# Performance work log

Hardware: AMD Instinct MI355X
Metric: run time of the kernel (lower is better)

The kernel has to match this reference:

```python
import jax, jax.numpy as jnp
import numpy as np

GROUPS = 8   # GroupNorm groups used by create_pat_conv*_blocks(..., groups=8)
EPS = 1e-5
K = 20       # num_neighbor


def group_norm(x, gamma, beta):
    # x: [B, C, ...spatial]
    B, C = x.shape[0], x.shape[1]
    shape = x.shape
    xg = x.reshape(B, GROUPS, C // GROUPS, -1)
    m = xg.mean(axis=(2, 3), keepdims=True)
    v = ((xg - m) ** 2).mean(axis=(2, 3), keepdims=True)
    xg = (xg - m) * jax.lax.rsqrt(v + EPS)
    x = xg.reshape(shape)
    bshape = (1, C) + (1,) * (len(shape) - 2)
    return x * gamma.reshape(bshape) + beta.reshape(bshape)


def conv_block(x, w, b, gamma, beta):
    # pointwise (kernel-size 1) conv + GroupNorm + ELU, works for 1d and 2d spatial
    y = jnp.einsum('oc,bc...->bo...', w, x) + b.reshape((1, -1) + (1,) * (x.ndim - 2))
    return jax.nn.elu(group_norm(y, gamma, beta))


def knn_graph(points, k):
    # points: [B, 3, N] -> neighbor coords [B, 3, N, k] (self included, dilation=1)
    sq = jnp.sum(points * points, axis=1)                      # [B, N]
    inner = jnp.einsum('bci,bcj->bij', points, points)         # [B, N, N]
    dist = sq[:, :, None] + sq[:, None, :] - 2.0 * inner       # squared pairwise dist
    _, idx = jax.lax.top_k(-dist, k)                           # [B, N, k] smallest dists
    neighbors = jnp.take_along_axis(points[:, :, None, :], idx[:, None, :, :], axis=3)
    return neighbors                                           # [B, 3, N, k]


def setup_inputs() -> dict:
    key = jax.random.key(0)
    B, N = 4, 8192
    dims1 = [6, 32, 64]
    dims2 = [64, 512, 1024]
    keys = iter(jax.random.split(key, 32))
    inp = {"points": jax.random.normal(next(keys), (B, 3, N), dtype=jnp.float32)}
    for tag, dims in (("p1", dims1), ("p2", dims2)):
        for i in range(len(dims) - 1):
            cin, cout = dims[i], dims[i + 1]
            inp[f"{tag}_w{i}"] = jax.random.normal(next(keys), (cout, cin), dtype=jnp.float32) / np.float32(np.sqrt(cin))
            inp[f"{tag}_b{i}"] = jnp.zeros((cout,), dtype=jnp.float32)
            inp[f"{tag}_g{i}"] = jnp.ones((cout,), dtype=jnp.float32)
            inp[f"{tag}_beta{i}"] = jnp.zeros((cout,), dtype=jnp.float32)
    return inp


def reference(points, p1_w0, p1_b0, p1_g0, p1_beta0, p1_w1, p1_b1, p1_g1, p1_beta1,
              p2_w0, p2_b0, p2_g0, p2_beta0, p2_w1, p2_b1, p2_g1, p2_beta1):
    neighbors = knn_graph(points, K)                             # [B, 3, N, K]
    center = jnp.broadcast_to(points[:, :, :, None], neighbors.shape)
    x = jnp.concatenate([center, neighbors - center], axis=1)   # [B, 6, N, K]
    x = conv_block(x, p1_w0, p1_b0, p1_g0, p1_beta0)            # [B, 32, N, K]
    x = conv_block(x, p1_w1, p1_b1, p1_g1, p1_beta1)            # [B, 64, N, K]
    x = jnp.max(x, axis=2)                                      # [B, 64, K] (faithful to source: max over dim=2)
    x = conv_block(x, p2_w0, p2_b0, p2_g0, p2_beta0)            # [B, 512, K]
    x = conv_block(x, p2_w1, p2_b1, p2_g1, p2_beta1)            # [B, 1024, K]
    return x
```

## Files before the change

kernel.cpp:

```cpp
#include <hip/hip_runtime.h>
#include <math.h>

#define NPTS   8192
#define BATCH  4
#define KNN    20
#define NKTOT  (NPTS*KNN)
#define EPS    1e-5f
#define FQC    64

#define WINW   3072
#define WITR   (WINW/4/128)
#define GWIN   2048
#define GITR   (GWIN/4/128)
#define NBIN   1024
#define BIN_LO (-4.5f)
#define BIN_W  (9.0f/1024.0f)

typedef float v2f __attribute__((ext_vector_type(2)));

__device__ __forceinline__ float elu(float x) { return x > 0.0f ? x : expm1f(x); }
__device__ __forceinline__ float eluf(float x) { return x > 0.0f ? x : __expf(x) - 1.0f; }
__device__ __forceinline__ v2f splat2(float x) { v2f v; v.x = x; v.y = x; return v; }
__device__ __forceinline__ float rfl(float x) {
    return __uint_as_float(__builtin_amdgcn_readfirstlane(__float_as_uint(x)));
}

__device__ __forceinline__ unsigned fenc(float f) {
    unsigned b = __float_as_uint(f);
    return b ^ ((unsigned)(((int)b) >> 31) | 0x80000000u);
}
__device__ __forceinline__ float fdec(unsigned u) {
    unsigned b = (u & 0x80000000u) ? (u ^ 0x80000000u) : ~u;
    return __uint_as_float(b);
}

__device__ __forceinline__ int xbin(float x) {
    int bin = (int)floorf((x + 4.5f) * (1024.0f / 9.0f));
    return bin < 0 ? 0 : (bin > NBIN - 1 ? NBIN - 1 : bin);
}

__device__ __forceinline__ unsigned long long packkey(float s, int orig, int slot) {
    return ((unsigned long long)fenc(s) << 32)
         | (unsigned)(((NPTS - 1 - orig) << 13) | slot);
}

__global__ __launch_bounds__(256) void prep_kernel(const float* __restrict__ points,
                                                   float4* __restrict__ pts4,
                                                   float* __restrict__ zeroreg,
                                                   unsigned* __restrict__ minenc,
                                                   unsigned* __restrict__ fcnt,
                                                   int* __restrict__ Pcur_part)
{
    __shared__ int lh[NBIN];
    const int t = blockIdx.x * 256 + threadIdx.x;
    const int b = t >> 13, n = t & (NPTS - 1);
    for (int i = threadIdx.x; i < NBIN; i += 256) lh[i] = 0;
    const float* px = points + b * 3 * NPTS;
    float x = px[n], y = px[NPTS + n], z = px[2 * NPTS + n];
    pts4[t] = make_float4(x, y, z, -0.5f * (x * x + y * y + z * z));
    if (t < 18176) zeroreg[t] = 0.f;
    if (t < 5120)  minenc[t] = 0xFFFFFFFFu;
    if (t < 4)     fcnt[t] = 0u;
    __syncthreads();
    atomicAdd(&lh[xbin(x)], 1);
    __syncthreads();
    for (int i = threadIdx.x; i < NBIN; i += 256)
        Pcur_part[blockIdx.x * NBIN + i] = lh[i];
}

__global__ __launch_bounds__(1024) void scan_kernel(const int* __restrict__ Pcur_part,
                                                    int* __restrict__ Pcur)
{
    __shared__ int sc[NBIN];
    const int b = blockIdx.x;
    const int t = threadIdx.x;
    int v = 0;
#pragma unroll 8
    for (int p = 0; p < 32; ++p)
        v += Pcur_part[(b * 32 + p) * NBIN + t];
    sc[t] = v;
    __syncthreads();
    for (int off = 1; off < NBIN; off <<= 1) {
        int a = (t >= off) ? sc[t - off] : 0;
        __syncthreads();
        sc[t] += a;
        __syncthreads();
    }
    Pcur[b * NBIN + t] = sc[t] - v;
}

__global__ __launch_bounds__(256) void scatter_kernel(const float4* __restrict__ pts4,
                                                      int* __restrict__ Pcur,
                                                      float4* __restrict__ psort,
                                                      int* __restrict__ sidx,
                                                      int* __restrict__ binof)
{
    const int t = blockIdx.x * 256 + threadIdx.x;
    const int b = t >> 13, n = t & (NPTS - 1);
    float4 p = pts4[t];
    int bin = xbin(p.x);
    int slot = atomicAdd(&Pcur[b * NBIN + bin], 1);
    psort[b * NPTS + slot] = p;
    sidx [b * NPTS + slot] = n;
    binof[b * NPTS + slot] = bin;
}

__global__ __launch_bounds__(256, 8) void knn_win_kernel(
    const float4* __restrict__ psort, const int* __restrict__ sidx,
    const int* __restrict__ binof, int* __restrict__ idx_out,
    unsigned* __restrict__ fcnt, int* __restrict__ flist)
{
    __shared__ unsigned long long queue[8][FQC];
    __shared__ float smaxs[4][8][64];
    __shared__ float gates[8];
    __shared__ int qcnt[8];

    const int tid  = threadIdx.x;
    const int lane = tid & 63;
    const int wv   = tid >> 6;
    const int b    = blockIdx.x >> 10;
    const int oct  = blockIdx.x & 1023;
    const int q0s  = oct * 8;
    const float4* psb = psort + b * NPTS;
    const int*    six = sidx  + b * NPTS;
    const int*    bob = binof + b * NPTS;

    int s = q0s + 4 - WINW / 2;
    if (s < 0) s = 0;
    if (s > NPTS - WINW) s = NPTS - WINW;
    int gs = q0s + 4 - GWIN / 2;
    if (gs < 0) gs = 0;
    if (gs > NPTS - GWIN) gs = NPTS - GWIN;

    if (tid < 8) qcnt[tid] = 0;

    float qx[8], qy[8], qz[8], q2[8];
    v2f smax2[8];
#pragma unroll
    for (int q = 0; q < 8; ++q) {
        float4 qp = psb[q0s + q];
        qx[q] = rfl(qp.x); qy[q] = rfl(qp.y); qz[q] = rfl(qp.z);
        q2[q] = rfl(-(qp.w + qp.w));
        smax2[q] = splat2(-INFINITY);
    }

    const int gbase = gs + (((lane >> 5) * 4 + wv) << 6) + ((lane & 31) << 1);
    const int lbase = s  + (((lane >> 5) * 4 + wv) << 6) + ((lane & 31) << 1);

#pragma unroll
    for (int t = 0; t < GITR; ++t) {
        float4 p0 = psb[gbase + t * 512];
        float4 p1 = psb[gbase + t * 512 + 1];
        v2f px = { p0.x, p1.x }, py = { p0.y, p1.y };
        v2f pz = { p0.z, p1.z }, pw = { p0.w, p1.w };
#pragma unroll
        for (int q = 0; q < 8; ++q) {
            v2f sv = __builtin_elementwise_fma(splat2(qx[q]), px,
                     __builtin_elementwise_fma(splat2(qy[q]), py,
                     __builtin_elementwise_fma(splat2(qz[q]), pz, pw)));
            smax2[q] = __builtin_elementwise_max(smax2[q], sv);
        }
    }
#pragma unroll
    for (int q = 0; q < 8; ++q) smaxs[wv][q][lane] = fmaxf(smax2[q].x, smax2[q].y);
    __syncthreads();

#pragma unroll
    for (int qq = 0; qq < 2; ++qq) {
        const int q = wv * 2 + qq;
        float v = fmaxf(fmaxf(smaxs[0][q][lane], smaxs[1][q][lane]),
                        fmaxf(smaxs[2][q][lane], smaxs[3][q][lane]));
#pragma unroll
        for (int k = 2; k <= 64; k <<= 1)
#pragma unroll
            for (int j = k >> 1; j >= 1; j >>= 1) {
                float o = __shfl_xor(v, j);
                bool up = ((lane & k) == 0);
                bool keepmin = (((lane & j) == 0) == up);
                v = keepmin ? fminf(v, o) : fmaxf(v, o);
            }
        float m = __shfl(v, 44);
        if (lane == 0) gates[q] = m - 1e-4f - 1e-5f * fabsf(m);
    }
    __syncthreads();
    float sgate[8];
#pragma unroll
    for (int q = 0; q < 8; ++q) sgate[q] = gates[q];

#pragma unroll
    for (int t = 0; t < WITR; ++t) {
        const int jb = lbase + t * 512;
        float4 p0 = psb[jb];
        float4 p1 = psb[jb + 1];
        v2f px = { p0.x, p1.x }, py = { p0.y, p1.y };
        v2f pz = { p0.z, p1.z }, pw = { p0.w, p1.w };
#pragma unroll
        for (int q = 0; q < 8; ++q) {
            v2f sv = __builtin_elementwise_fma(splat2(qx[q]), px,
                     __builtin_elementwise_fma(splat2(qy[q]), py,
                     __builtin_elementwise_fma(splat2(qz[q]), pz, pw)));
            if (fmaxf(sv.x, sv.y) >= sgate[q]) {
#pragma unroll
                for (int h = 0; h < 2; ++h) {
                    float svh = h ? sv.y : sv.x;
                    if (svh >= sgate[q]) {
                        int slot = atomicAdd(&qcnt[q], 1);
                        if (slot < FQC)
                            queue[q][slot] = packkey(svh, six[jb + h], jb + h);
                    }
                }
            }
        }
    }
    __syncthreads();

    float xLe = (s == 0) ? -3.0e38f
                         : (BIN_LO + (float)(bob[s] + 1) * BIN_W);
    float xRe = (s == NPTS - WINW) ? 3.0e38f
                         : (BIN_LO + (float)bob[s + WINW] * BIN_W);

#pragma unroll
    for (int qq = 0; qq < 2; ++qq) {
        const int q = wv * 2 + qq;
        const int cr = qcnt[q];
        const bool ovf = (cr > FQC);
        const int c = cr < FQC ? cr : FQC;
        unsigned long long key = (lane < c) ? queue[q][lane] : 0ull;
#pragma unroll
        for (int k = 2; k <= 64; k <<= 1)
#pragma unroll
            for (int j = k >> 1; j >= 1; j >>= 1) {
                unsigned long long o = __shfl_xor(key, j);
                bool up = ((lane & k) == 0);
                bool keepmax = (((lane & j) == 0) == up);
                bool omax = o > key;
                key = (keepmax == omax) ? o : key;
            }
        if (lane < KNN)
            idx_out[(b * KNN + lane) * NPTS + (q0s + q)] =
                (int)(unsigned)(key & 0x1FFFu);

        unsigned long long k19 = __shfl(key, 19);
        float s20 = fdec((unsigned)(k19 >> 32));
        float d20 = fmaxf(q2[q] - 2.0f * s20, 0.0f);
        float mg  = 1e-3f + 1e-3f * d20;
        float dL  = qx[q] - xLe;
        float dR  = xRe - qx[q];
        bool ok = !ovf && (c >= KNN) && dL > 0.0f && dR > 0.0f
                  && (d20 + mg < dL * dL) && (d20 + mg < dR * dR);
        if (!ok && lane == 0) {
            unsigned fs = atomicAdd(&fcnt[b], 1u);
            if (fs < 8192u) flist[b * 8192 + fs] = q0s + q;
        }
    }
}

__global__ __launch_bounds__(256, 8) void knn_fb_kernel(const float4* __restrict__ psort,
                                                        const int* __restrict__ sidx,
                                                        int* __restrict__ idx_out,
                                                        const unsigned* __restrict__ fcnt,
                                                        const int* __restrict__ flist)
{
    __shared__ unsigned long long queue[2][FQC];
    __shared__ float smaxs[4][2][64];
    __shared__ float gates[2];
    __shared__ int qcnt[2];

    const int tid  = threadIdx.x;
    const int lane = tid & 63;
    const int wv   = tid >> 6;
    const int bb   = blockIdx.x & 3;
    unsigned cnt = fcnt[bb];
    if (cnt > 8192u) cnt = 8192u;
    if (cnt == 0u) return;
    const float4* pb = psort + bb * NPTS;
    const int* six = sidx + bb * NPTS;
    const int* fl = flist + bb * 8192;
    const int cbase = wv * (NPTS / 4);
    const int tstep = gridDim.x >> 2;

    for (int task = blockIdx.x >> 2; task * 2 < (int)cnt; task += tstep) {
        int qs[2];
        float qx[2], qy[2], qz[2];
        v2f smax2[2];
        if (tid < 2) qcnt[tid] = 0;
#pragma unroll
        for (int q = 0; q < 2; ++q) {
            int e = task * 2 + q;
            if (e >= (int)cnt) e = (int)cnt - 1;
            qs[q] = __builtin_amdgcn_readfirstlane(fl[e]);
            float4 qp = pb[qs[q]];
            qx[q] = rfl(qp.x); qy[q] = rfl(qp.y); qz[q] = rfl(qp.z);
            smax2[q] = splat2(-INFINITY);
        }

#pragma unroll 4
        for (int t = 0; t < NPTS / 4 / 128; ++t) {
            float4 p0 = pb[cbase + t * 128 + 2 * lane];
            float4 p1 = pb[cbase + t * 128 + 2 * lane + 1];
            v2f px = { p0.x, p1.x }, py = { p0.y, p1.y };
            v2f pz = { p0.z, p1.z }, pw = { p0.w, p1.w };
#pragma unroll
            for (int q = 0; q < 2; ++q) {
                v2f sv = __builtin_elementwise_fma(splat2(qx[q]), px,
                         __builtin_elementwise_fma(splat2(qy[q]), py,
                         __builtin_elementwise_fma(splat2(qz[q]), pz, pw)));
                smax2[q] = __builtin_elementwise_max(smax2[q], sv);
            }
        }
#pragma unroll
        for (int q = 0; q < 2; ++q) smaxs[wv][q][lane] = fmaxf(smax2[q].x, smax2[q].y);
        __syncthreads();

        if (wv < 2) {
            const int q = wv;
            float v = fmaxf(fmaxf(smaxs[0][q][lane], smaxs[1][q][lane]),
                            fmaxf(smaxs[2][q][lane], smaxs[3][q][lane]));
#pragma unroll
            for (int k = 2; k <= 64; k <<= 1)
#pragma unroll
                for (int j = k >> 1; j >= 1; j >>= 1) {
                    float o = __shfl_xor(v, j);
                    bool up = ((lane & k) == 0);
                    bool keepmin = (((lane & j) == 0) == up);
                    v = keepmin ? fminf(v, o) : fmaxf(v, o);
                }
            float m = __shfl(v, 44);
            if (lane == 0) gates[q] = m - 1e-4f - 1e-5f * fabsf(m);
        }
        __syncthreads();
        float sg0 = gates[0], sg1 = gates[1];

        for (int t = 0; t < NPTS / 4 / 128; ++t) {
            const int jb = cbase + t * 128 + 2 * lane;
            float4 p0 = pb[jb];
            float4 p1 = pb[jb + 1];
            v2f px = { p0.x, p1.x }, py = { p0.y, p1.y };
            v2f pz = { p0.z, p1.z }, pw = { p0.w, p1.w };
#pragma unroll
            for (int q = 0; q < 2; ++q) {
                float sg = q ? sg1 : sg0;
                v2f sv = __builtin_elementwise_fma(splat2(qx[q]), px,
                         __builtin_elementwise_fma(splat2(qy[q]), py,
                         __builtin_elementwise_fma(splat2(qz[q]), pz, pw)));
                if (fmaxf(sv.x, sv.y) >= sg) {
#pragma unroll
                    for (int h = 0; h < 2; ++h) {
                        float svh = h ? sv.y : sv.x;
                        if (svh >= sg) {
                            int slot = atomicAdd(&qcnt[q], 1);
                            if (slot < FQC)
                                queue[q][slot] = packkey(svh, six[jb + h], jb + h);
                        }
                    }
                }
            }
        }
        __syncthreads();

        if (wv < 2) {
            const int q = wv;
            int c = qcnt[q]; c = c < FQC ? c : FQC;
            unsigned long long key = (lane < c) ? queue[q][lane] : 0ull;
#pragma unroll
            for (int k = 2; k <= 64; k <<= 1)
#pragma unroll
                for (int j = k >> 1; j >= 1; j >>= 1) {
                    unsigned long long o = __shfl_xor(key, j);
                    bool up = ((lane & k) == 0);
                    bool keepmax = (((lane & j) == 0) == up);
                    bool omax = o > key;
                    key = (keepmax == omax) ? o : key;
                }
            if (lane < KNN)
                idx_out[(bb * KNN + lane) * NPTS + qs[q]] =
                    (int)(unsigned)(key & 0x1FFFu);
        }
        __syncthreads();
    }
}

__global__ __launch_bounds__(256) void moments_x_kernel(const float4* __restrict__ psort,
                                                        const int* __restrict__ idx,
                                                        float* __restrict__ sums1p)
{
    const int b  = blockIdx.x / 80;
    const int r0 = (blockIdx.x - b * 80) * 2048;
    const float4* pb = psort + b * NPTS;
    const int* ib = idx + b * NKTOT;

    float v[27];
#pragma unroll
    for (int i = 0; i < 27; ++i) v[i] = 0.f;

    for (int e = 0; e < 8; ++e) {
        const int id = r0 + e * 256 + threadIdx.x;
        const int n = id & (NPTS - 1);
        const int j = ib[id];
        float4 c4 = pb[n];
        float4 e4 = pb[j];
        float x[6] = { c4.x, c4.y, c4.z, e4.x - c4.x, e4.y - c4.y, e4.z - c4.z };
        int p = 6;
#pragma unroll
        for (int d = 0; d < 6; ++d) {
            v[d] += x[d];
#pragma unroll
            for (int ee = d; ee < 6; ++ee) v[p++] += x[d] * x[ee];
        }
    }
#pragma unroll
    for (int i = 0; i < 27; ++i)
        for (int o = 32; o > 0; o >>= 1) v[i] += __shfl_xor(v[i], o);

    __shared__ float red[4][27];
    const int lane = threadIdx.x & 63, w = threadIdx.x >> 6;
    if (lane == 0)
#pragma unroll
        for (int i = 0; i < 27; ++i) red[w][i] = v[i];
    __syncthreads();
    if (threadIdx.x < 27) {
        float acc = red[0][threadIdx.x] + red[1][threadIdx.x] + red[2][threadIdx.x] + red[3][threadIdx.x];
        int slot = blockIdx.x & 63;
        atomicAdd(&sums1p[(slot * BATCH + b) * 27 + threadIdx.x], acc);
    }
}

__global__ void finalize1_kernel(const float* __restrict__ sums1p,
                                 const float* __restrict__ w1, const float* __restrict__ b1,
                                 const float* __restrict__ g1, const float* __restrict__ beta1,
                                 float* __restrict__ w1f)
{
    __shared__ float S[BATCH][27];
    const int t = threadIdx.x;
    if (t < 108) {
        int b = t / 27, i = t % 27;
        float acc = 0.f;
        for (int s = 0; s < 64; ++s) acc += sums1p[(s * BATCH + b) * 27 + i];
        S[b][i] = acc;
    }
    __syncthreads();
    const int b = t >> 5, c = t & 31;
    const float invS = 1.0f / (float)NKTOT;
    float Ex[6], M[6][6];
#pragma unroll
    for (int d = 0; d < 6; ++d) Ex[d] = S[b][d] * invS;
    int p = 6;
#pragma unroll
    for (int d = 0; d < 6; ++d)
#pragma unroll
        for (int e = d; e < 6; ++e) { float v = S[b][p++] * invS; M[d][e] = v; M[e][d] = v; }
    const int g = c >> 2;
    float msum = 0.f, qsum = 0.f;
    for (int cc = g * 4; cc < g * 4 + 4; ++cc) {
        float w[6];
#pragma unroll
        for (int d = 0; d < 6; ++d) w[d] = w1[cc * 6 + d];
        float dotEx = 0.f;
#pragma unroll
        for (int d = 0; d < 6; ++d) dotEx += w[d] * Ex[d];
        float Ey = dotEx + b1[cc];
        float Ey2 = 0.f;
#pragma unroll
        for (int d = 0; d < 6; ++d)
#pragma unroll
            for (int e = 0; e < 6; ++e) Ey2 += w[d] * w[e] * M[d][e];
        Ey2 += 2.0f * b1[cc] * dotEx + b1[cc] * b1[cc];
        msum += Ey; qsum += Ey2;
    }
    float m = msum * 0.25f;
    float var = qsum * 0.25f - m * m;
    float inv = rsqrtf(var + EPS);
    float s = g1[c] * inv;
    float tt = s * (b1[c] - m) + beta1[c];
    float* o = w1f + (b * 32 + c) * 8;
#pragma unroll
    for (int d = 0; d < 6; ++d) o[d] = s * w1[c * 6 + d];
    o[6] = tt; o[7] = 0.f;
}

__global__ __launch_bounds__(256, 3) void fused_main_kernel(
    const float4* __restrict__ psort, const int* __restrict__ idxb,
    const float* __restrict__ w1f, const float* __restrict__ w2, const float* __restrict__ b2,
    float* __restrict__ sums2p, unsigned int* __restrict__ maxenc, unsigned int* __restrict__ minenc)
{
    __shared__ __align__(16) float w2t[32 * 64];
    __shared__ __align__(16) float z1s[32 * 256];
    __shared__ __align__(16) float4 w1s4[64];
    __shared__ float b2s[64];
    __shared__ float redmx[256], redmn[256], sqred[64];

    const int t   = threadIdx.x;
    const int blk = blockIdx.x;
    const int nc  = blk & 15;
    const int k   = (blk >> 4) % 20;
    const int b   = blk / 320;

    for (int i = t; i < 512; i += 256) {
        float4 v = ((const float4*)w2)[i];
        int c = i >> 3, kq = (i & 7) * 4;
        w2t[(kq + 0) * 64 + c] = v.x; w2t[(kq + 1) * 64 + c] = v.y;
        w2t[(kq + 2) * 64 + c] = v.z; w2t[(kq + 3) * 64 + c] = v.w;
    }
    if (t < 64) { w1s4[t] = ((const float4*)w1f)[b * 64 + t]; b2s[t] = b2[t]; }

    const int wvi = t >> 6;
    const int cg8 = t & 7;
    const int n0  = (t >> 3) * 8;
    const int c0  = cg8 * 8;
    const float4* pb = psort + b * NPTS;
    const int nbase = nc * 512;
    const int* idxrow = idxb + (b * KNN + k) * NPTS;

    float mx[8], mn[8];
#pragma unroll
    for (int ci = 0; ci < 8; ++ci) { mx[ci] = -INFINITY; mn[ci] = INFINITY; }
    float gs = 0.f, gq = 0.f;

    for (int ph = 0; ph < 2; ++ph) {
        const int n = nbase + ph * 256 + t;
        const int j = idxrow[n];
        float4 c4 = pb[n];
        float4 e4 = pb[j];
        float x0[6] = { c4.x, c4.y, c4.z, e4.x - c4.x, e4.y - c4.y, e4.z - c4.z };

        __syncthreads();
#pragma unroll
        for (int c = 0; c < 32; ++c) {
            float4 wA = w1s4[c * 2 + 0];
            float4 wB = w1s4[c * 2 + 1];
            float z = wB.z;
            z = fmaf(wA.x, x0[0], z); z = fmaf(wA.y, x0[1], z); z = fmaf(wA.z, x0[2], z);
            z = fmaf(wA.w, x0[3], z); z = fmaf(wB.x, x0[4], z); z = fmaf(wB.y, x0[5], z);
            z1s[c * 256 + t] = eluf(z);
        }
        __syncthreads();

        float acc[8][8];
#pragma unroll
        for (int ci = 0; ci < 8; ++ci) {
            float bb = b2s[c0 + ci];
#pragma unroll
            for (int pj = 0; pj < 8; ++pj) acc[ci][pj] = bb;
        }
#pragma unroll
        for (int kk = 0; kk < 32; ++kk) {
            float4 a0 = *(const float4*)&w2t[kk * 64 + c0];
            float4 a1 = *(const float4*)&w2t[kk * 64 + c0 + 4];
            float4 z0 = *(const float4*)&z1s[kk * 256 + n0];
            float4 z1v = *(const float4*)&z1s[kk * 256 + n0 + 4];
            float avv[8] = { a0.x, a0.y, a0.z, a0.w, a1.x, a1.y, a1.z, a1.w };
            float zvv[8] = { z0.x, z0.y, z0.z, z0.w, z1v.x, z1v.y, z1v.z, z1v.w };
#pragma unroll
            for (int ci = 0; ci < 8; ++ci)
#pragma unroll
                for (int pj = 0; pj < 8; ++pj) acc[ci][pj] = fmaf(avv[ci], zvv[pj], acc[ci][pj]);
        }
#pragma unroll
        for (int ci = 0; ci < 8; ++ci)
#pragma unroll
            for (int pj = 0; pj < 8; ++pj) {
                float v = acc[ci][pj];
                gs += v; gq = fmaf(v, v, gq);
                mx[ci] = fmaxf(mx[ci], v); mn[ci] = fminf(mn[ci], v);
            }
    }

#pragma unroll
    for (int m = 8; m <= 32; m <<= 1) {
#pragma unroll
        for (int ci = 0; ci < 8; ++ci) {
            mx[ci] = fmaxf(mx[ci], __shfl_xor(mx[ci], m));
            mn[ci] = fminf(mn[ci], __shfl_xor(mn[ci], m));
        }
        gs += __shfl_xor(gs, m);
        gq += __shfl_xor(gq, m);
    }
    if ((t & 63) < 8) {
        const int l = t & 7;
#pragma unroll
        for (int ci = 0; ci < 8; ++ci) {
            redmx[wvi * 64 + l * 8 + ci] = mx[ci];
            redmn[wvi * 64 + l * 8 + ci] = mn[ci];
        }
        sqred[(wvi * 8 + l) * 2 + 0] = gs;
        sqred[(wvi * 8 + l) * 2 + 1] = gq;
    }
    __syncthreads();
    if (t < 64) {
        float m = fmaxf(fmaxf(redmx[t], redmx[64 + t]), fmaxf(redmx[128 + t], redmx[192 + t]));
        atomicMax(&maxenc[(b * 64 + t) * KNN + k], fenc(m));
    } else if (t < 128) {
        int c = t - 64;
        float m = fminf(fminf(redmn[c], redmn[64 + c]), fminf(redmn[128 + c], redmn[192 + c]));
        atomicMin(&minenc[(b * 64 + c) * KNN + k], fenc(m));
    } else if (t < 144) {
        int i2 = t - 128, g = i2 >> 1, w = i2 & 1;
        float v = 0.f;
#pragma unroll
        for (int wv2 = 0; wv2 < 4; ++wv2)
            v += sqred[(wv2 * 8 + g) * 2 + w];
        int slot = blk & 63;
        atomicAdd(&sums2p[((slot * BATCH + b) * 8 + g) * 2 + w], v);
    }
}

__global__ void build_m1_kernel(const float* __restrict__ sums2p,
                                const unsigned int* __restrict__ maxenc,
                                const unsigned int* __restrict__ minenc,
                                const float* __restrict__ gamma, const float* __restrict__ beta,
                                float* __restrict__ m1)
{
    const int t = blockIdx.x * 256 + threadIdx.x;
    const int b = t / 1280;
    const int r = t - b * 1280;
    const int c = r / 20;
    const int g = c >> 3;
    float s = 0.f, q = 0.f;
    for (int sl = 0; sl < 64; ++sl) {
        s += sums2p[((sl * BATCH + b) * 8 + g) * 2 + 0];
        q += sums2p[((sl * BATCH + b) * 8 + g) * 2 + 1];
    }
    const float cnt = 8.0f * (float)NKTOT;
    float m = s / cnt;
    float var = q / cnt - m * m;
    float inv = rsqrtf(var + EPS);
    float sc = gamma[c] * inv;
    float tt = beta[c] - sc * m;
    float y = (sc >= 0.f) ? fdec(maxenc[t]) : fdec(minenc[t]);
    m1[t] = elu(sc * y + tt);
}

template <int CIN, int SLOTS>
__global__ void p2_gemm_kernel(const float* __restrict__ zin, const float* __restrict__ w,
                               const float* __restrict__ bias, float* __restrict__ yout,
                               float* __restrict__ sumsp, int chans_per_group)
{
    const int t = blockIdx.x * 256 + threadIdx.x;
    const int per_b = (gridDim.x * 256) / BATCH;
    const int b = t / per_b;
    const int r = t - b * per_b;
    const int o = r / 20;
    const int k = r - o * 20;
    const float* zb = zin + b * CIN * 20;
    const float* wrow = w + o * CIN;
    float acc = bias[o];
    for (int c = 0; c < CIN; c += 4) {
        float4 wv = *(const float4*)&wrow[c];
        acc += wv.x * zb[(c + 0) * 20 + k] + wv.y * zb[(c + 1) * 20 + k]
             + wv.z * zb[(c + 2) * 20 + k] + wv.w * zb[(c + 3) * 20 + k];
    }
    yout[t] = acc;

    __shared__ float ls[16];
    if (threadIdx.x < 16) ls[threadIdx.x] = 0.f;
    __syncthreads();
    const int g = o / chans_per_group;
    atomicAdd(&ls[g * 2 + 0], acc);
    atomicAdd(&ls[g * 2 + 1], acc * acc);
    __syncthreads();
    if (threadIdx.x < 16) {
        int slot = blockIdx.x & (SLOTS - 1);
        atomicAdd(&sumsp[(slot * BATCH + b) * 16 + threadIdx.x], ls[threadIdx.x]);
    }
}

template <int SLOTS>
__global__ void p2_finalize_kernel(const float* __restrict__ y, const float* __restrict__ sumsp,
                                   const float* __restrict__ gamma, const float* __restrict__ beta,
                                   float* __restrict__ z, int chans_per_group, float cnt)
{
    const int t = blockIdx.x * 256 + threadIdx.x;
    const int per_b = (gridDim.x * 256) / BATCH;
    const int b = t / per_b;
    const int r = t - b * per_b;
    const int o = r / 20;
    const int g = o / chans_per_group;
    float s = 0.f, q = 0.f;
    for (int sl = 0; sl < SLOTS; ++sl) {
        s += sumsp[(sl * BATCH + b) * 16 + g * 2 + 0];
        q += sumsp[(sl * BATCH + b) * 16 + g * 2 + 1];
    }
    float m = s / cnt;
    float var = q / cnt - m * m;
    float inv = rsqrtf(var + EPS);
    float v = gamma[o] * inv * (y[t] - m) + beta[o];
    z[t] = elu(v);
}

extern "C" void kernel_launch(void* const* d_in, const int* in_sizes, int n_in,
                              void* d_out, int out_size, void* d_ws, size_t ws_size,
                              hipStream_t stream)
{
    const float* points  = (const float*)d_in[0];
    const float* p1_w0   = (const float*)d_in[1];
    const float* p1_b0   = (const float*)d_in[2];
    const float* p1_g0   = (const float*)d_in[3];
    const float* p1_bt0  = (const float*)d_in[4];
    const float* p1_w1   = (const float*)d_in[5];
    const float* p1_b1   = (const float*)d_in[6];
    const float* p1_g1   = (const float*)d_in[7];
    const float* p1_bt1  = (const float*)d_in[8];
    const float* p2_w0   = (const float*)d_in[9];
    const float* p2_b0   = (const float*)d_in[10];
    const float* p2_g0   = (const float*)d_in[11];
    const float* p2_bt0  = (const float*)d_in[12];
    const float* p2_w1   = (const float*)d_in[13];
    const float* p2_b1   = (const float*)d_in[14];
    const float* p2_g1   = (const float*)d_in[15];
    const float* p2_bt1  = (const float*)d_in[16];
    float* out = (float*)d_out;

    float* ws = (float*)d_ws;
    int*      idx     = (int*)ws;
    float*    sums1p  = ws + 655360;
    float*    sums2p  = sums1p + 6912;
    float*    sumsAp  = sums2p + 4096;
    float*    sumsBp  = sumsAp + 1024;
    unsigned* maxenc  = (unsigned*)(sumsBp + 1024);
    unsigned* minenc  = maxenc + 5120;
    float*    w1f     = (float*)(minenc + 5120);
    float*    m1      = w1f + 1024;
    float*    yp2a    = m1 + 5120;
    float*    zp2a    = yp2a + 40960;
    float*    yp2b    = zp2a + 40960;
    float4*   pts4    = (float4*)yp2a;
    int*      Pcur_part = idx;
    float*    psortf  = yp2b + 81920;
    float4*   psort4  = (float4*)psortf;
    int*      sidx    = (int*)(psortf + 131072);
    int*      binof   = sidx + 32768;
    int*      Pcur    = binof + 32768 + 64;
    unsigned* fcnt4   = (unsigned*)(Pcur + 4096);
    int*      flist   = (int*)(fcnt4 + 64);

    prep_kernel<<<128, 256, 0, stream>>>(points, pts4, sums1p, minenc, fcnt4, Pcur_part);
    scan_kernel<<<4, 1024, 0, stream>>>(Pcur_part, Pcur);
    scatter_kernel<<<128, 256, 0, stream>>>(pts4, Pcur, psort4, sidx, binof);
    knn_win_kernel<<<4096, 256, 0, stream>>>(psort4, sidx, binof, idx, fcnt4, flist);
    knn_fb_kernel<<<4096, 256, 0, stream>>>(psort4, sidx, idx, fcnt4, flist);
    moments_x_kernel<<<320, 256, 0, stream>>>(psort4, idx, sums1p);
    finalize1_kernel<<<1, 128, 0, stream>>>(sums1p, p1_w0, p1_b0, p1_g0, p1_bt0, w1f);
    fused_main_kernel<<<1280, 256, 0, stream>>>(psort4, idx, w1f, p1_w1, p1_b1,
                                                sums2p, maxenc, minenc);
    build_m1_kernel<<<20, 256, 0, stream>>>(sums2p, maxenc, minenc, p1_g1, p1_bt1, m1);
    p2_gemm_kernel<64, 16><<<160, 256, 0, stream>>>(m1, p2_w0, p2_b0, yp2a, sumsAp, 64);
    p2_finalize_kernel<16><<<160, 256, 0, stream>>>(yp2a, sumsAp, p2_g0, p2_bt0, zp2a, 64, 1280.0f);
    p2_gemm_kernel<512, 16><<<320, 256, 0, stream>>>(zp2a, p2_w1, p2_b1, yp2b, sumsBp, 128);
    p2_finalize_kernel<16><<<320, 256, 0, stream>>>(yp2b, sumsBp, p2_g1, p2_bt1, out, 128, 2560.0f);
}
```

Before: 268.9 us.

## Fold scan and finalize kernels into neighbors via last-block counters; shrink KNN window

The histogram scan moves into the scatter kernel: each block recomputes the global prefix offsets from the per-block histograms and ranks its points through shared-memory atomics. finalize1 and build_m1 become last-block epilogues of moments_x and fused_main, driven by atomic counters and thread fences. This removes three kernel launches and their serialization gaps. Separately, the KNN window shrinks from 3072 to 2048 and reuses the gate window, which cuts candidate work but may push more queries onto the fallback path. The last-block tails run serially on a single block.

```diff
diff --git a/kernel.cpp b/kernel.cpp
--- a/kernel.cpp
+++ b/kernel.cpp
@@ -8,10 +8,8 @@
 #define EPS    1e-5f
 #define FQC    64
 
-#define WINW   3072
+#define WINW   2048
 #define WITR   (WINW/4/128)
-#define GWIN   2048
-#define GITR   (GWIN/4/128)
 #define NBIN   1024
 #define BIN_LO (-4.5f)
 #define BIN_W  (9.0f/1024.0f)
@@ -60,7 +58,7 @@
     pts4[t] = make_float4(x, y, z, -0.5f * (x * x + y * y + z * z));
     if (t < 18176) zeroreg[t] = 0.f;
     if (t < 5120)  minenc[t] = 0xFFFFFFFFu;
-    if (t < 4)     fcnt[t] = 0u;
+    if (t < 8)     fcnt[t] = 0u;
     __syncthreads();
     atomicAdd(&lh[xbin(x)], 1);
     __syncthreads();
@@ -68,38 +66,48 @@
         Pcur_part[blockIdx.x * NBIN + i] = lh[i];
 }
 
-__global__ __launch_bounds__(1024) void scan_kernel(const int* __restrict__ Pcur_part,
-                                                    int* __restrict__ Pcur)
-{
-    __shared__ int sc[NBIN];
-    const int b = blockIdx.x;
-    const int t = threadIdx.x;
-    int v = 0;
-#pragma unroll 8
-    for (int p = 0; p < 32; ++p)
-        v += Pcur_part[(b * 32 + p) * NBIN + t];
-    sc[t] = v;
-    __syncthreads();
-    for (int off = 1; off < NBIN; off <<= 1) {
-        int a = (t >= off) ? sc[t - off] : 0;
-        __syncthreads();
-        sc[t] += a;
-        __syncthreads();
-    }
-    Pcur[b * NBIN + t] = sc[t] - v;
-}
-
 __global__ __launch_bounds__(256) void scatter_kernel(const float4* __restrict__ pts4,
-                                                      int* __restrict__ Pcur,
+                                                      const int* __restrict__ Pcur_part,
                                                       float4* __restrict__ psort,
                                                       int* __restrict__ sidx,
                                                       int* __restrict__ binof)
 {
-    const int t = blockIdx.x * 256 + threadIdx.x;
-    const int b = t >> 13, n = t & (NPTS - 1);
-    float4 p = pts4[t];
+    __shared__ int boff[NBIN];
+    __shared__ int brank[NBIN];
+    __shared__ int wsum[256];
+    const int jb = blockIdx.x & 31;
+    const int b  = blockIdx.x >> 5;
+    const int tt = threadIdx.x;
+    const int t0 = tt * 4;
+
+    int tot0 = 0, tot1 = 0, tot2 = 0, tot3 = 0;
+    int pre0 = 0, pre1 = 0, pre2 = 0, pre3 = 0;
+    for (int p = 0; p < 32; ++p) {
+        const int4 c = *(const int4*)&Pcur_part[(b * 32 + p) * NBIN + t0];
+        tot0 += c.x; tot1 += c.y; tot2 += c.z; tot3 += c.w;
+        if (p < jb) { pre0 += c.x; pre1 += c.y; pre2 += c.z; pre3 += c.w; }
+    }
+    const int tsum = tot0 + tot1 + tot2 + tot3;
+    wsum[tt] = tsum;
+    __syncthreads();
+    for (int off = 1; off < 256; off <<= 1) {
+        int a = (tt >= off) ? wsum[tt - off] : 0;
+        __syncthreads();
+        wsum[tt] += a;
+        __syncthreads();
+    }
+    int run = wsum[tt] - tsum;
+    boff[t0 + 0] = run + pre0; run += tot0;
+    boff[t0 + 1] = run + pre1; run += tot1;
+    boff[t0 + 2] = run + pre2; run += tot2;
+    boff[t0 + 3] = run + pre3;
+    for (int i = tt; i < NBIN; i += 256) brank[i] = 0;
+    __syncthreads();
+
+    const int n = jb * 256 + tt;
+    float4 p = pts4[b * NPTS + n];
     int bin = xbin(p.x);
-    int slot = atomicAdd(&Pcur[b * NBIN + bin], 1);
+    int slot = boff[bin] + atomicAdd(&brank[bin], 1);
     psort[b * NPTS + slot] = p;
     sidx [b * NPTS + slot] = n;
     binof[b * NPTS + slot] = bin;
@@ -128,9 +136,6 @@
     int s = q0s + 4 - WINW / 2;
     if (s < 0) s = 0;
     if (s > NPTS - WINW) s = NPTS - WINW;
-    int gs = q0s + 4 - GWIN / 2;
-    if (gs < 0) gs = 0;
-    if (gs > NPTS - GWIN) gs = NPTS - GWIN;
 
     if (tid < 8) qcnt[tid] = 0;
 
@@ -144,13 +149,12 @@
         smax2[q] = splat2(-INFINITY);
     }
 
-    const int gbase = gs + (((lane >> 5) * 4 + wv) << 6) + ((lane & 31) << 1);
-    const int lbase = s  + (((lane >> 5) * 4 + wv) << 6) + ((lane & 31) << 1);
-
-#pragma unroll
-    for (int t = 0; t < GITR; ++t) {
-        float4 p0 = psb[gbase + t * 512];
-        float4 p1 = psb[gbase + t * 512 + 1];
+    const int lbase = s + (((lane >> 5) * 4 + wv) << 6) + ((lane & 31) << 1);
+
+#pragma unroll
+    for (int t = 0; t < WITR; ++t) {
+        float4 p0 = psb[lbase + t * 512];
+        float4 p1 = psb[lbase + t * 512 + 1];
         v2f px = { p0.x, p1.x }, py = { p0.y, p1.y };
         v2f pz = { p0.z, p1.z }, pw = { p0.w, p1.w };
 #pragma unroll
@@ -382,7 +386,13 @@
 
 __global__ __launch_bounds__(256) void moments_x_kernel(const float4* __restrict__ psort,
                                                         const int* __restrict__ idx,
-                                                        float* __restrict__ sums1p)
+                                                        float* __restrict__ sums1p,
+                                                        const float* __restrict__ w1,
+                                                        const float* __restrict__ b1,
+                                                        const float* __restrict__ g1,
+                                                        const float* __restrict__ beta1,
+                                                        float* __restrict__ w1f,
+                                                        unsigned* __restrict__ ctr)
 {
     const int b  = blockIdx.x / 80;
     const int r0 = (blockIdx.x - b * 80) * 2048;
@@ -423,65 +433,71 @@
         int slot = blockIdx.x & 63;
         atomicAdd(&sums1p[(slot * BATCH + b) * 27 + threadIdx.x], acc);
     }
-}
-
-__global__ void finalize1_kernel(const float* __restrict__ sums1p,
-                                 const float* __restrict__ w1, const float* __restrict__ b1,
-                                 const float* __restrict__ g1, const float* __restrict__ beta1,
-                                 float* __restrict__ w1f)
-{
+
+    __threadfence();
+    __syncthreads();
+    __shared__ int lastm;
+    if (threadIdx.x == 0) lastm = (atomicAdd(ctr, 1u) == 319u) ? 1 : 0;
+    __syncthreads();
+    if (!lastm) return;
+    __threadfence();
+
     __shared__ float S[BATCH][27];
     const int t = threadIdx.x;
     if (t < 108) {
-        int b = t / 27, i = t % 27;
+        int bb = t / 27, i = t % 27;
         float acc = 0.f;
-        for (int s = 0; s < 64; ++s) acc += sums1p[(s * BATCH + b) * 27 + i];
-        S[b][i] = acc;
-    }
-    __syncthreads();
-    const int b = t >> 5, c = t & 31;
-    const float invS = 1.0f / (float)NKTOT;
-    float Ex[6], M[6][6];
-#pragma unroll
-    for (int d = 0; d < 6; ++d) Ex[d] = S[b][d] * invS;
-    int p = 6;
-#pragma unroll
-    for (int d = 0; d < 6; ++d)
-#pragma unroll
-        for (int e = d; e < 6; ++e) { float v = S[b][p++] * invS; M[d][e] = v; M[e][d] = v; }
-    const int g = c >> 2;
-    float msum = 0.f, qsum = 0.f;
-    for (int cc = g * 4; cc < g * 4 + 4; ++cc) {
-        float w[6];
-#pragma unroll
-        for (int d = 0; d < 6; ++d) w[d] = w1[cc * 6 + d];
-        float dotEx = 0.f;
-#pragma unroll
-        for (int d = 0; d < 6; ++d) dotEx += w[d] * Ex[d];
-        float Ey = dotEx + b1[cc];
-        float Ey2 = 0.f;
+        for (int s = 0; s < 64; ++s) acc += sums1p[(s * BATCH + bb) * 27 + i];
+        S[bb][i] = acc;
+    }
+    __syncthreads();
+    if (t < 128) {
+        const int bb = t >> 5, c = t & 31;
+        const float invS = 1.0f / (float)NKTOT;
+        float Ex[6], M[6][6];
+#pragma unroll
+        for (int d = 0; d < 6; ++d) Ex[d] = S[bb][d] * invS;
+        int p = 6;
 #pragma unroll
         for (int d = 0; d < 6; ++d)
 #pragma unroll
-            for (int e = 0; e < 6; ++e) Ey2 += w[d] * w[e] * M[d][e];
-        Ey2 += 2.0f * b1[cc] * dotEx + b1[cc] * b1[cc];
-        msum += Ey; qsum += Ey2;
-    }
-    float m = msum * 0.25f;
-    float var = qsum * 0.25f - m * m;
-    float inv = rsqrtf(var + EPS);
-    float s = g1[c] * inv;
-    float tt = s * (b1[c] - m) + beta1[c];
-    float* o = w1f + (b * 32 + c) * 8;
-#pragma unroll
-    for (int d = 0; d < 6; ++d) o[d] = s * w1[c * 6 + d];
-    o[6] = tt; o[7] = 0.f;
+            for (int e = d; e < 6; ++e) { float vv = S[bb][p++] * invS; M[d][e] = vv; M[e][d] = vv; }
+        const int g = c >> 2;
+        float msum = 0.f, qsum = 0.f;
+        for (int cc = g * 4; cc < g * 4 + 4; ++cc) {
+            float wv[6];
+#pragma unroll
+            for (int d = 0; d < 6; ++d) wv[d] = w1[cc * 6 + d];
+            float dotEx = 0.f;
+#pragma unroll
+            for (int d = 0; d < 6; ++d) dotEx += wv[d] * Ex[d];
+            float Ey = dotEx + b1[cc];
+            float Ey2 = 0.f;
+#pragma unroll
+            for (int d = 0; d < 6; ++d)
+#pragma unroll
+                for (int e = 0; e < 6; ++e) Ey2 += wv[d] * wv[e] * M[d][e];
+            Ey2 += 2.0f * b1[cc] * dotEx + b1[cc] * b1[cc];
+            msum += Ey; qsum += Ey2;
+        }
+        float m = msum * 0.25f;
+        float var = qsum * 0.25f - m * m;
+        float inv = rsqrtf(var + EPS);
+        float sca = g1[c] * inv;
+        float tt2 = sca * (b1[c] - m) + beta1[c];
+        float* o = w1f + (bb * 32 + c) * 8;
+#pragma unroll
+        for (int d = 0; d < 6; ++d) o[d] = sca * w1[c * 6 + d];
+        o[6] = tt2; o[7] = 0.f;
+    }
 }
 
 __global__ __launch_bounds__(256, 3) void fused_main_kernel(
     const float4* __restrict__ psort, const int* __restrict__ idxb,
     const float* __restrict__ w1f, const float* __restrict__ w2, const float* __restrict__ b2,
-    float* __restrict__ sums2p, unsigned int* __restrict__ maxenc, unsigned int* __restrict__ minenc)
+    float* __restrict__ sums2p, unsigned int* __restrict__ maxenc, unsigned int* __restrict__ minenc,
+    const float* __restrict__ gamma2, const float* __restrict__ beta2,
+    float* __restrict__ m1, unsigned* __restrict__ ctr)
 {
     __shared__ __align__(16) float w2t[32 * 64];
     __shared__ __align__(16) float z1s[32 * 256];
@@ -602,32 +618,38 @@
         int slot = blk & 63;
         atomicAdd(&sums2p[((slot * BATCH + b) * 8 + g) * 2 + w], v);
     }
-}
-
-__global__ void build_m1_kernel(const float* __restrict__ sums2p,
-                                const unsigned int* __restrict__ maxenc,
-                                const unsigned int* __restrict__ minenc,
-                                const float* __restrict__ gamma, const float* __restrict__ beta,
-                                float* __restrict__ m1)
-{
-    const int t = blockIdx.x * 256 + threadIdx.x;
-    const int b = t / 1280;
-    const int r = t - b * 1280;
-    const int c = r / 20;
-    const int g = c >> 3;
-    float s = 0.f, q = 0.f;
-    for (int sl = 0; sl < 64; ++sl) {
-        s += sums2p[((sl * BATCH + b) * 8 + g) * 2 + 0];
-        q += sums2p[((sl * BATCH + b) * 8 + g) * 2 + 1];
-    }
+
+    __threadfence();
+    __syncthreads();
+    __shared__ int lastf;
+    if (t == 0) lastf = (atomicAdd(ctr, 1u) == 1279u) ? 1 : 0;
+    __syncthreads();
+    if (!lastf) return;
+    __threadfence();
+
+    __shared__ float smv[4][8][2];
+    if (t < 64) {
+        int bb = t >> 4, g = (t >> 1) & 7, w = t & 1;
+        float a = 0.f;
+        for (int sl = 0; sl < 64; ++sl)
+            a += sums2p[((sl * BATCH + bb) * 8 + g) * 2 + w];
+        smv[bb][g][w] = a;
+    }
+    __syncthreads();
     const float cnt = 8.0f * (float)NKTOT;
-    float m = s / cnt;
-    float var = q / cnt - m * m;
-    float inv = rsqrtf(var + EPS);
-    float sc = gamma[c] * inv;
-    float tt = beta[c] - sc * m;
-    float y = (sc >= 0.f) ? fdec(maxenc[t]) : fdec(minenc[t]);
-    m1[t] = elu(sc * y + tt);
+    for (int i = t; i < BATCH * 64 * KNN; i += 256) {
+        const int bb = i / 1280;
+        const int r = i - bb * 1280;
+        const int c = r / 20;
+        const int g = c >> 3;
+        float m = smv[bb][g][0] / cnt;
+        float var = smv[bb][g][1] / cnt - m * m;
+        float inv = rsqrtf(var + EPS);
+        float sc = gamma2[c] * inv;
+        float tt2 = beta2[c] - sc * m;
+        float y = (sc >= 0.f) ? fdec(maxenc[i]) : fdec(minenc[i]);
+        m1[i] = elu(sc * y + tt2);
+    }
 }
 
 template <int CIN, int SLOTS>
@@ -729,20 +751,18 @@
     float4*   psort4  = (float4*)psortf;
     int*      sidx    = (int*)(psortf + 131072);
     int*      binof   = sidx + 32768;
-    int*      Pcur    = binof + 32768 + 64;
-    unsigned* fcnt4   = (unsigned*)(Pcur + 4096);
-    int*      flist   = (int*)(fcnt4 + 64);
-
-    prep_kernel<<<128, 256, 0, stream>>>(points, pts4, sums1p, minenc, fcnt4, Pcur_part);
-    scan_kernel<<<4, 1024, 0, stream>>>(Pcur_part, Pcur);
-    scatter_kernel<<<128, 256, 0, stream>>>(pts4, Pcur, psort4, sidx, binof);
-    knn_win_kernel<<<4096, 256, 0, stream>>>(psort4, sidx, binof, idx, fcnt4, flist);
-    knn_fb_kernel<<<4096, 256, 0, stream>>>(psort4, sidx, idx, fcnt4, flist);
-    moments_x_kernel<<<320, 256, 0, stream>>>(psort4, idx, sums1p);
-    finalize1_kernel<<<1, 128, 0, stream>>>(sums1p, p1_w0, p1_b0, p1_g0, p1_bt0, w1f);
+    unsigned* fcnt8   = (unsigned*)(binof + 32768 + 64);
+    int*      flist   = (int*)(fcnt8 + 64);
+
+    prep_kernel<<<128, 256, 0, stream>>>(points, pts4, sums1p, minenc, fcnt8, Pcur_part);
+    scatter_kernel<<<128, 256, 0, stream>>>(pts4, Pcur_part, psort4, sidx, binof);
+    knn_win_kernel<<<4096, 256, 0, stream>>>(psort4, sidx, binof, idx, fcnt8, flist);
+    knn_fb_kernel<<<4096, 256, 0, stream>>>(psort4, sidx, idx, fcnt8, flist);
+    moments_x_kernel<<<320, 256, 0, stream>>>(psort4, idx, sums1p,
+                                              p1_w0, p1_b0, p1_g0, p1_bt0, w1f, fcnt8 + 4);
     fused_main_kernel<<<1280, 256, 0, stream>>>(psort4, idx, w1f, p1_w1, p1_b1,
-                                                sums2p, maxenc, minenc);
-    build_m1_kernel<<<20, 256, 0, stream>>>(sums2p, maxenc, minenc, p1_g1, p1_bt1, m1);
+                                                sums2p, maxenc, minenc,
+                                                p1_g1, p1_bt1, m1, fcnt8 + 5);
     p2_gemm_kernel<64, 16><<<160, 256, 0, stream>>>(m1, p2_w0, p2_b0, yp2a, sumsAp, 64);
     p2_finalize_kernel<16><<<160, 256, 0, stream>>>(yp2a, sumsAp, p2_g0, p2_bt0, zp2a, 64, 1280.0f);
     p2_gemm_kernel<512, 16><<<320, 256, 0, stream>>>(zp2a, p2_w1, p2_b1, yp2b, sumsBp, 128);
```

New measurement: 415.1 us. 54.4% more time.

## Fold bin prefix scan into scatter and shrink KNN candidate window

Applied to the files above, without the earlier changes.

Removes the separate scan kernel launch. Each scatter block now recomputes the per-batch bin prefix sums from the partial histograms and ranks its own points with shared-memory atomics. The KNN window kernel drops the separate gate window and uses one 2048-point window for both the gate and the candidate scan, which cuts per-query distance work. A smaller window can send more queries to the fallback kernel, and the fallback counter array is widened to 8 entries. Every scatter block also redundantly reads 32 histogram rows.

```diff
diff --git a/kernel.cpp b/kernel.cpp
--- a/kernel.cpp
+++ b/kernel.cpp
@@ -8,10 +8,8 @@
 #define EPS    1e-5f
 #define FQC    64
 
-#define WINW   3072
+#define WINW   2048
 #define WITR   (WINW/4/128)
-#define GWIN   2048
-#define GITR   (GWIN/4/128)
 #define NBIN   1024
 #define BIN_LO (-4.5f)
 #define BIN_W  (9.0f/1024.0f)
@@ -60,7 +58,7 @@
     pts4[t] = make_float4(x, y, z, -0.5f * (x * x + y * y + z * z));
     if (t < 18176) zeroreg[t] = 0.f;
     if (t < 5120)  minenc[t] = 0xFFFFFFFFu;
-    if (t < 4)     fcnt[t] = 0u;
+    if (t < 8)     fcnt[t] = 0u;
     __syncthreads();
     atomicAdd(&lh[xbin(x)], 1);
     __syncthreads();
@@ -68,38 +66,48 @@
         Pcur_part[blockIdx.x * NBIN + i] = lh[i];
 }
 
-__global__ __launch_bounds__(1024) void scan_kernel(const int* __restrict__ Pcur_part,
-                                                    int* __restrict__ Pcur)
-{
-    __shared__ int sc[NBIN];
-    const int b = blockIdx.x;
-    const int t = threadIdx.x;
-    int v = 0;
-#pragma unroll 8
-    for (int p = 0; p < 32; ++p)
-        v += Pcur_part[(b * 32 + p) * NBIN + t];
-    sc[t] = v;
-    __syncthreads();
-    for (int off = 1; off < NBIN; off <<= 1) {
-        int a = (t >= off) ? sc[t - off] : 0;
-        __syncthreads();
-        sc[t] += a;
-        __syncthreads();
-    }
-    Pcur[b * NBIN + t] = sc[t] - v;
-}
-
 __global__ __launch_bounds__(256) void scatter_kernel(const float4* __restrict__ pts4,
-                                                      int* __restrict__ Pcur,
+                                                      const int* __restrict__ Pcur_part,
                                                       float4* __restrict__ psort,
                                                       int* __restrict__ sidx,
                                                       int* __restrict__ binof)
 {
-    const int t = blockIdx.x * 256 + threadIdx.x;
-    const int b = t >> 13, n = t & (NPTS - 1);
-    float4 p = pts4[t];
+    __shared__ int boff[NBIN];
+    __shared__ int brank[NBIN];
+    __shared__ int wsum[256];
+    const int jb = blockIdx.x & 31;
+    const int b  = blockIdx.x >> 5;
+    const int tt = threadIdx.x;
+    const int t0 = tt * 4;
+
+    int tot0 = 0, tot1 = 0, tot2 = 0, tot3 = 0;
+    int pre0 = 0, pre1 = 0, pre2 = 0, pre3 = 0;
+    for (int p = 0; p < 32; ++p) {
+        const int4 c = *(const int4*)&Pcur_part[(b * 32 + p) * NBIN + t0];
+        tot0 += c.x; tot1 += c.y; tot2 += c.z; tot3 += c.w;
+        if (p < jb) { pre0 += c.x; pre1 += c.y; pre2 += c.z; pre3 += c.w; }
+    }
+    const int tsum = tot0 + tot1 + tot2 + tot3;
+    wsum[tt] = tsum;
+    __syncthreads();
+    for (int off = 1; off < 256; off <<= 1) {
+        int a = (tt >= off) ? wsum[tt - off] : 0;
+        __syncthreads();
+        wsum[tt] += a;
+        __syncthreads();
+    }
+    int run = wsum[tt] - tsum;
+    boff[t0 + 0] = run + pre0; run += tot0;
+    boff[t0 + 1] = run + pre1; run += tot1;
+    boff[t0 + 2] = run + pre2; run += tot2;
+    boff[t0 + 3] = run + pre3;
+    for (int i = tt; i < NBIN; i += 256) brank[i] = 0;
+    __syncthreads();
+
+    const int n = jb * 256 + tt;
+    float4 p = pts4[b * NPTS + n];
     int bin = xbin(p.x);
-    int slot = atomicAdd(&Pcur[b * NBIN + bin], 1);
+    int slot = boff[bin] + atomicAdd(&brank[bin], 1);
     psort[b * NPTS + slot] = p;
     sidx [b * NPTS + slot] = n;
     binof[b * NPTS + slot] = bin;
@@ -128,9 +136,6 @@
     int s = q0s + 4 - WINW / 2;
     if (s < 0) s = 0;
     if (s > NPTS - WINW) s = NPTS - WINW;
-    int gs = q0s + 4 - GWIN / 2;
-    if (gs < 0) gs = 0;
-    if (gs > NPTS - GWIN) gs = NPTS - GWIN;
 
     if (tid < 8) qcnt[tid] = 0;
 
@@ -144,13 +149,12 @@
         smax2[q] = splat2(-INFINITY);
     }
 
-    const int gbase = gs + (((lane >> 5) * 4 + wv) << 6) + ((lane & 31) << 1);
-    const int lbase = s  + (((lane >> 5) * 4 + wv) << 6) + ((lane & 31) << 1);
-
-#pragma unroll
-    for (int t = 0; t < GITR; ++t) {
-        float4 p0 = psb[gbase + t * 512];
-        float4 p1 = psb[gbase + t * 512 + 1];
+    const int lbase = s + (((lane >> 5) * 4 + wv) << 6) + ((lane & 31) << 1);
+
+#pragma unroll
+    for (int t = 0; t < WITR; ++t) {
+        float4 p0 = psb[lbase + t * 512];
+        float4 p1 = psb[lbase + t * 512 + 1];
         v2f px = { p0.x, p1.x }, py = { p0.y, p1.y };
         v2f pz = { p0.z, p1.z }, pw = { p0.w, p1.w };
 #pragma unroll
@@ -729,15 +733,13 @@
     float4*   psort4  = (float4*)psortf;
     int*      sidx    = (int*)(psortf + 131072);
     int*      binof   = sidx + 32768;
-    int*      Pcur    = binof + 32768 + 64;
-    unsigned* fcnt4   = (unsigned*)(Pcur + 4096);
-    int*      flist   = (int*)(fcnt4 + 64);
-
-    prep_kernel<<<128, 256, 0, stream>>>(points, pts4, sums1p, minenc, fcnt4, Pcur_part);
-    scan_kernel<<<4, 1024, 0, stream>>>(Pcur_part, Pcur);
-    scatter_kernel<<<128, 256, 0, stream>>>(pts4, Pcur, psort4, sidx, binof);
-    knn_win_kernel<<<4096, 256, 0, stream>>>(psort4, sidx, binof, idx, fcnt4, flist);
-    knn_fb_kernel<<<4096, 256, 0, stream>>>(psort4, sidx, idx, fcnt4, flist);
+    unsigned* fcnt8   = (unsigned*)(binof + 32768 + 64);
+    int*      flist   = (int*)(fcnt8 + 64);
+
+    prep_kernel<<<128, 256, 0, stream>>>(points, pts4, sums1p, minenc, fcnt8, Pcur_part);
+    scatter_kernel<<<128, 256, 0, stream>>>(pts4, Pcur_part, psort4, sidx, binof);
+    knn_win_kernel<<<4096, 256, 0, stream>>>(psort4, sidx, binof, idx, fcnt8, flist);
+    knn_fb_kernel<<<4096, 256, 0, stream>>>(psort4, sidx, idx, fcnt8, flist);
     moments_x_kernel<<<320, 256, 0, stream>>>(psort4, idx, sums1p);
     finalize1_kernel<<<1, 128, 0, stream>>>(sums1p, p1_w0, p1_b0, p1_g0, p1_bt0, w1f);
     fused_main_kernel<<<1280, 256, 0, stream>>>(psort4, idx, w1f, p1_w1, p1_b1,
```

After: 333.1 us. +23.9%, slower.
